# Optimization experiments

Measured on AMD Instinct MI355X. Metric: run time of the kernel, lower is better.

Reference implementation:

```python
import jax, jax.numpy as jnp
import numpy as np

N_OBJ, IN_DIM, MID_DIM, OUT_DIM = 2048, 128, 256, 1


def setup_inputs() -> dict:
    key = jax.random.key(0)
    ks = jax.random.split(key, 7)
    s = 0.05  # keep sigmoid inputs in a sane range
    return {
        "x": jax.random.normal(ks[0], (N_OBJ, IN_DIM), dtype=jnp.float32),
        "W1": jax.random.normal(ks[1], (N_OBJ, MID_DIM, IN_DIM), dtype=jnp.float32) * s,
        "b1": jax.random.normal(ks[2], (N_OBJ, MID_DIM), dtype=jnp.float32) * s,
        "W2": jax.random.normal(ks[3], (N_OBJ, MID_DIM, MID_DIM), dtype=jnp.float32) * s,
        "b2": jax.random.normal(ks[4], (N_OBJ, MID_DIM), dtype=jnp.float32) * s,
        "W3": jax.random.normal(ks[5], (N_OBJ, OUT_DIM, MID_DIM), dtype=jnp.float32) * s,
        "b3": jax.random.normal(ks[6], (N_OBJ, OUT_DIM), dtype=jnp.float32) * s,
    }


def reference(x, W1, b1, W2, b2, W3, b3):
    # Per-object 3-layer MLP, batched as grouped GEMV over the object axis.
    # NOTE: faithful to original — NO activation after fc1.
    y1 = jnp.einsum("oi,omi->om", x, W1) + b1            # [O, mid]
    y2 = jax.nn.sigmoid(jnp.einsum("om,onm->on", y1, W2) + b2)  # [O, mid]
    y3 = jax.nn.sigmoid(jnp.einsum("on,okn->ok", y2, W3) + b3)  # [O, 1]
    return y3[:, 0]  # [n_objects]
```

## Files before the change

### kernel.cpp

```cpp
#include <hip/hip_runtime.h>
#include <math.h>


#define N_OBJ   2048
#define IN_DIM  128
#define MID_DIM 256

__global__ __launch_bounds__(256, 8) void mlp_grouped_kernel(
    const float* __restrict__ x,
    const float* __restrict__ W1,
    const float* __restrict__ b1,
    const float* __restrict__ W2,
    const float* __restrict__ b2,
    const float* __restrict__ W3,
    const float* __restrict__ b3,
    float* __restrict__ out)
{
    const int o = blockIdx.x;
    const int t = threadIdx.x;

    __shared__ __align__(16) float s_x[IN_DIM];
    __shared__ __align__(16) float s_y1[MID_DIM];
    __shared__ __align__(16) float s_y2[MID_DIM];
    __shared__ float s_red[4];

    if (t < IN_DIM) s_x[t] = x[(size_t)o * IN_DIM + t];
    __syncthreads();

    {
        const float4* w = (const float4*)(W1 + (size_t)o * MID_DIM * IN_DIM
                                             + (size_t)t * IN_DIM);
        const float4* xv = (const float4*)s_x;
        float acc = 0.0f;
        #pragma unroll 8
        for (int j = 0; j < IN_DIM / 4; ++j) {
            float4 wv = w[j];
            float4 v  = xv[j];
            acc += wv.x * v.x + wv.y * v.y + wv.z * v.z + wv.w * v.w;
        }
        s_y1[t] = acc + b1[(size_t)o * MID_DIM + t];
    }
    __syncthreads();

    {
        const float4* w = (const float4*)(W2 + (size_t)o * MID_DIM * MID_DIM
                                             + (size_t)t * MID_DIM);
        const float4* yv = (const float4*)s_y1;
        float acc = 0.0f;
        #pragma unroll 8
        for (int j = 0; j < MID_DIM / 4; ++j) {
            float4 wv = w[j];
            float4 v  = yv[j];
            acc += wv.x * v.x + wv.y * v.y + wv.z * v.z + wv.w * v.w;
        }
        acc += b2[(size_t)o * MID_DIM + t];
        s_y2[t] = 1.0f / (1.0f + expf(-acc));
    }
    __syncthreads();

    {
        float p = s_y2[t] * W3[(size_t)o * MID_DIM + t];
        #pragma unroll
        for (int off = 32; off > 0; off >>= 1)
            p += __shfl_down(p, off, 64);
        if ((t & 63) == 0) s_red[t >> 6] = p;
        __syncthreads();
        if (t == 0) {
            float s = s_red[0] + s_red[1] + s_red[2] + s_red[3]
                    + b3[o];
            out[o] = 1.0f / (1.0f + expf(-s));
        }
    }
}

extern "C" void kernel_launch(void* const* d_in, const int* in_sizes, int n_in,
                              void* d_out, int out_size, void* d_ws, size_t ws_size,
                              hipStream_t stream) {
    const float* x  = (const float*)d_in[0];
    const float* W1 = (const float*)d_in[1];
    const float* b1 = (const float*)d_in[2];
    const float* W2 = (const float*)d_in[3];
    const float* b2 = (const float*)d_in[4];
    const float* W3 = (const float*)d_in[5];
    const float* b3 = (const float*)d_in[6];
    float* out = (float*)d_out;

    mlp_grouped_kernel<<<N_OBJ, 256, 0, stream>>>(x, W1, b1, W2, b2, W3, b3, out);
}
```

Measured before the change: 838.9 us.

## Coalesce weight reads by assigning lanes across row columns with shuffle reductions

```diff
diff --git a/kernel.cpp b/kernel.cpp
--- a/kernel.cpp
+++ b/kernel.cpp
@@ -18,57 +18,70 @@
 {
     const int o = blockIdx.x;
     const int t = threadIdx.x;
+    const int w = t >> 6;
+    const int l = t & 63;
 
-    __shared__ __align__(16) float s_x[IN_DIM];
     __shared__ __align__(16) float s_y1[MID_DIM];
     __shared__ __align__(16) float s_y2[MID_DIM];
-    __shared__ float s_red[4];
-
-    if (t < IN_DIM) s_x[t] = x[(size_t)o * IN_DIM + t];
-    __syncthreads();
 
     {
-        const float4* w = (const float4*)(W1 + (size_t)o * MID_DIM * IN_DIM
-                                             + (size_t)t * IN_DIM);
-        const float4* xv = (const float4*)s_x;
-        float acc = 0.0f;
-        #pragma unroll 8
-        for (int j = 0; j < IN_DIM / 4; ++j) {
-            float4 wv = w[j];
-            float4 v  = xv[j];
-            acc += wv.x * v.x + wv.y * v.y + wv.z * v.z + wv.w * v.w;
+        const int sub = l & 31;
+        const int rh  = l >> 5;
+        const float4 xv = *(const float4*)(x + (size_t)o * IN_DIM + sub * 4);
+        const float* W1o = W1 + (size_t)o * MID_DIM * IN_DIM;
+
+        #pragma unroll 4
+        for (int i = 0; i < 32; ++i) {
+            const int row = w * 64 + 2 * i + rh;
+            float4 wv = *(const float4*)(W1o + (size_t)row * IN_DIM + sub * 4);
+            float acc = wv.x * xv.x + wv.y * xv.y + wv.z * xv.z + wv.w * xv.w;
+            acc += __shfl_xor(acc, 16, 32);
+            acc += __shfl_xor(acc,  8, 32);
+            acc += __shfl_xor(acc,  4, 32);
+            acc += __shfl_xor(acc,  2, 32);
+            acc += __shfl_xor(acc,  1, 32);
+            if (sub == 0)
+                s_y1[row] = acc + b1[(size_t)o * MID_DIM + row];
         }
-        s_y1[t] = acc + b1[(size_t)o * MID_DIM + t];
     }
     __syncthreads();
 
     {
-        const float4* w = (const float4*)(W2 + (size_t)o * MID_DIM * MID_DIM
-                                             + (size_t)t * MID_DIM);
-        const float4* yv = (const float4*)s_y1;
-        float acc = 0.0f;
-        #pragma unroll 8
-        for (int j = 0; j < MID_DIM / 4; ++j) {
-            float4 wv = w[j];
-            float4 v  = yv[j];
-            acc += wv.x * v.x + wv.y * v.y + wv.z * v.z + wv.w * v.w;
+        const float4 yv = *(const float4*)(s_y1 + l * 4);
+        const float* W2o = W2 + (size_t)o * MID_DIM * MID_DIM;
+
+        #pragma unroll 4
+        for (int i = 0; i < 64; ++i) {
+            const int row = w * 64 + i;
+            float4 wv = *(const float4*)(W2o + (size_t)row * MID_DIM + l * 4);
+            float acc = wv.x * yv.x + wv.y * yv.y + wv.z * yv.z + wv.w * yv.w;
+            acc += __shfl_xor(acc, 32, 64);
+            acc += __shfl_xor(acc, 16, 64);
+            acc += __shfl_xor(acc,  8, 64);
+            acc += __shfl_xor(acc,  4, 64);
+            acc += __shfl_xor(acc,  2, 64);
+            acc += __shfl_xor(acc,  1, 64);
+            if (l == 0) {
+                float z = acc + b2[(size_t)o * MID_DIM + row];
+                s_y2[row] = 1.0f / (1.0f + expf(-z));
+            }
         }
-        acc += b2[(size_t)o * MID_DIM + t];
-        s_y2[t] = 1.0f / (1.0f + expf(-acc));
     }
     __syncthreads();
 
-    {
-        float p = s_y2[t] * W3[(size_t)o * MID_DIM + t];
-        #pragma unroll
-        for (int off = 32; off > 0; off >>= 1)
-            p += __shfl_down(p, off, 64);
-        if ((t & 63) == 0) s_red[t >> 6] = p;
-        __syncthreads();
-        if (t == 0) {
-            float s = s_red[0] + s_red[1] + s_red[2] + s_red[3]
-                    + b3[o];
-            out[o] = 1.0f / (1.0f + expf(-s));
+    if (w == 0) {
+        const float4 yv = *(const float4*)(s_y2 + l * 4);
+        const float4 wv = *(const float4*)(W3 + (size_t)o * MID_DIM + l * 4);
+        float acc = wv.x * yv.x + wv.y * yv.y + wv.z * yv.z + wv.w * yv.w;
+        acc += __shfl_xor(acc, 32, 64);
+        acc += __shfl_xor(acc, 16, 64);
+        acc += __shfl_xor(acc,  8, 64);
+        acc += __shfl_xor(acc,  4, 64);
+        acc += __shfl_xor(acc,  2, 64);
+        acc += __shfl_xor(acc,  1, 64);
+        if (l == 0) {
+            float z = acc + b3[o];
+            out[o] = 1.0f / (1.0f + expf(-z));
         }
     }
 }
```

After: 835.6 us. No clear change (-0.4%).
